# Optimization experiments

Hardware: AMD Instinct MI355X
Metric: run time of the kernel (lower is better)

Reference implementation:

```python
import jax, jax.numpy as jnp
import numpy as np
from jax.scipy.linalg import expm

U_SHAPE = (4, 32, 16, 16, 16, 3, 3)   # [mu, t, x, y, z, 3, 3]
W_SHAPE = (8, 32, 16, 16, 16, 3, 3)   # [feature, t, x, y, z, 3, 3]


def setup_inputs() -> dict:
    key = jax.random.key(0)
    k = jax.random.split(key, 5)
    return {
        "U_re": jax.random.normal(k[0], U_SHAPE, jnp.float32),
        "U_im": jax.random.normal(k[1], U_SHAPE, jnp.float32),
        "W_re": jax.random.normal(k[2], W_SHAPE, jnp.float32),
        "W_im": jax.random.normal(k[3], W_SHAPE, jnp.float32),
        "ah_weights": jax.random.normal(k[4], (4, W_SHAPE[0]), jnp.float32),
    }


def reference(U_re, U_im, W_re, W_im, ah_weights):
    U = (U_re + 1j * U_im).astype(jnp.complex64)
    W = (W_re + 1j * W_im).astype(jnp.complex64)

    # anti-hermitian part: W - W^dagger
    W_adj = jnp.conj(jnp.swapaxes(W, -1, -2))
    A = W - W_adj
    # traceless projection
    tr = jnp.trace(A, axis1=-2, axis2=-1)  # [i,t,x,y,z]
    A = A - (tr / 3.0)[..., None, None] * jnp.eye(3, dtype=A.dtype)

    # exponent: (1j*w) contracted with (-1j*A) == w contracted with A
    E = jnp.einsum('ui,itxyzab->utxyzab', ah_weights.astype(A.dtype), A)

    # batched 3x3 matrix exponential over the whole lattice
    E_flat = E.reshape(-1, 3, 3)
    expE = jax.vmap(expm)(E_flat).reshape(E.shape)

    # apply to gauge links: exp(...) @ U
    return jnp.einsum('utxyzij,utxyzjk->utxyzik', expE, U)
```

## Files before the change

kernel.cpp:

```cpp
#include <hip/hip_runtime.h>
#include <math.h>

#define NSITES 131072
#define HALFS  (NSITES / 2)
#define PL     (NSITES * 9)

struct cplx { float re, im; };

__device__ __forceinline__ cplx cadd(cplx a, cplx b) { return {a.re + b.re, a.im + b.im}; }
__device__ __forceinline__ cplx cmul(cplx a, cplx b) {
    return { fmaf(a.re, b.re, -(a.im * b.im)), fmaf(a.re, b.im, a.im * b.re) };
}

struct __attribute__((aligned(4))) f3 { float x, y, z; };
__device__ __forceinline__ f3 ld3(const float* __restrict__ p) { return *(const f3*)p; }
__device__ __forceinline__ void ld9(const float* __restrict__ p, float* r) {
    f3 a = *(const f3*)p, b = *(const f3*)(p + 3), c = *(const f3*)(p + 6);
    r[0] = a.x; r[1] = a.y; r[2] = a.z;
    r[3] = b.x; r[4] = b.y; r[5] = b.z;
    r[6] = c.x; r[7] = c.y; r[8] = c.z;
}

template<int IMM>
__device__ __forceinline__ void accf(const float* a, float wf, float* acc) {
    #pragma unroll
    for (int m = 0; m < 9; m++)
        acc[m] = fmaf(wf,
            __int_as_float(__builtin_amdgcn_ds_swizzle(__float_as_int(a[m]), IMM)),
            acc[m]);
}

__device__ __forceinline__ void prered(f3 q, f3 s, const float* wi, float* fr) {
    fr[0] = q.x - q.z;     fr[1] = q.y - s.y;     fr[2] = s.x - s.z;
    fr[3] = wi[1] + wi[3]; fr[4] = wi[2] + wi[6]; fr[5] = wi[5] + wi[7];
    fr[6] = wi[0];         fr[7] = wi[4];         fr[8] = wi[8];
}

struct Edof { float er01, er02, er12, ei01, ei02, ei12, ed0, ed1, ed2; };

__device__ __forceinline__ Edof make_edof(const float* acc) {
    Edof E;
    E.er01 = acc[0]; E.er02 = acc[1]; E.er12 = acc[2];
    E.ei01 = acc[3]; E.ei02 = acc[4]; E.ei12 = acc[5];
    float t3 = (acc[6] + acc[7] + acc[8]) * (2.f / 3.f);
    E.ed0 = fmaf(2.f, acc[6], -t3);
    E.ed1 = fmaf(2.f, acc[7], -t3);
    E.ed2 = fmaf(2.f, acc[8], -t3);
    return E;
}

__device__ __forceinline__ void expm_coeffs(const Edof& E, cplx& g0o, cplx& g1o, cplx& g2o)
{
    float r2 = fmaf(E.er01, E.er01, fmaf(E.er02, E.er02, fmaf(E.er12, E.er12,
               fmaf(E.ei01, E.ei01, fmaf(E.ei02, E.ei02, E.ei12 * E.ei12)))));
    r2 = fmaf(2.f, r2, fmaf(E.ed0, E.ed0, fmaf(E.ed1, E.ed1, E.ed2 * E.ed2)));

    const float n01 = fmaf(E.ei01, E.ei01, E.er01 * E.er01);
    const float n02 = fmaf(E.ei02, E.ei02, E.er02 * E.er02);
    const float n12 = fmaf(E.ei12, E.ei12, E.er12 * E.er12);
    const float zre = fmaf(E.ei01, E.ei12, -(E.er01 * E.er12));
    const float zim = -fmaf(E.ei01, E.er12, E.er01 * E.ei12);
    const float detH = E.ed0 * E.ed1 * E.ed2
                     + 2.f * fmaf(zre, E.ei02, -(zim * E.er02))
                     - fmaf(E.ed0, n12, fmaf(E.ed1, n02, E.ed2 * n01));

    int e; (void)frexpf(r2, &e);
    int sc = (e <= -2) ? 0 : min(1 + ((e + 1) >> 1), 40);
    const float inv  = __int_as_float((127 - sc) << 23);
    const float inv2 = inv * inv;
    const float px   = -0.5f * r2 * inv2;
    const float qxi  = -detH * (inv2 * inv);

    cplx T0 = {1.f, 0.f}, T1 = {0.f, 0.f}, T2 = {0.f, 0.f};
    cplx S0 = {1.f, 0.f}, S1 = {0.f, 0.f}, S2 = {0.f, 0.f};
    #pragma unroll
    for (int n = 1; n <= 10; n++) {
        float c  = 1.f / (float)n;
        float qc = qxi * c;
        cplx nT0 = { -qc * T2.im, qc * T2.re };
        cplx nT1 = { c * fmaf(px, T2.re, T0.re), c * fmaf(px, T2.im, T0.im) };
        cplx nT2 = { c * T1.re, c * T1.im };
        T0 = nT0; T1 = nT1; T2 = nT2;
        S0 = cadd(S0, T0); S1 = cadd(S1, T1); S2 = cadd(S2, T2);
    }

    const float q2 = 2.f * qxi;
    for (int k = 0; k < sc; k++) {
        cplx f0 = S0, f1 = S1, f2 = S2;
        cplx f12 = cmul(f1, f2);
        cplx f01 = cmul(f0, f1);
        cplx f02 = cmul(f0, f2);
        float f00re = fmaf(f0.re, f0.re, -(f0.im * f0.im)), f00im = 2.f * f0.re * f0.im;
        float f11re = fmaf(f1.re, f1.re, -(f1.im * f1.im)), f11im = 2.f * f1.re * f1.im;
        float f22re = fmaf(f2.re, f2.re, -(f2.im * f2.im)), f22im = 2.f * f2.re * f2.im;
        S0.re = fmaf(-q2, f12.im, f00re);
        S0.im = fmaf( q2, f12.re, f00im);
        S1.re = fmaf(-qxi, f22im, 2.f * fmaf(px, f12.re, f01.re));
        S1.im = fmaf( qxi, f22re, 2.f * fmaf(px, f12.im, f01.im));
        S2.re = fmaf(px, f22re, fmaf(2.f, f02.re, f11re));
        S2.im = fmaf(px, f22im, fmaf(2.f, f02.im, f11im));
    }
    g0o = S0;
    g1o = { S1.re * inv,  S1.im * inv  };
    g2o = { S2.re * inv2, S2.im * inv2 };
}

__device__ __forceinline__ void ecol(const Edof& E, cplx m0, cplx m1, cplx m2,
                                     cplx& v0, cplx& v1, cplx& v2)
{
    v0.re = fmaf(-E.ed0, m0.im, fmaf(E.er01, m1.re, fmaf(-E.ei01, m1.im, fmaf(E.er02, m2.re, -(E.ei02 * m2.im)))));
    v0.im = fmaf( E.ed0, m0.re, fmaf(E.er01, m1.im, fmaf( E.ei01, m1.re, fmaf(E.er02, m2.im,  (E.ei02 * m2.re)))));
    v1.re = fmaf(-E.er01, m0.re, fmaf(-E.ei01, m0.im, fmaf(-E.ed1, m1.im, fmaf(E.er12, m2.re, -(E.ei12 * m2.im)))));
    v1.im = fmaf(-E.er01, m0.im, fmaf( E.ei01, m0.re, fmaf( E.ed1, m1.re, fmaf(E.er12, m2.im,  (E.ei12 * m2.re)))));
    v2.re = fmaf(-E.er02, m0.re, fmaf(-E.ei02, m0.im, fmaf(-E.er12, m1.re, fmaf(-E.ei12, m1.im, -(E.ed2 * m2.im)))));
    v2.im = fmaf(-E.er02, m0.im, fmaf( E.ei02, m0.re, fmaf(-E.er12, m1.im, fmaf( E.ei12, m1.re,  (E.ed2 * m2.re)))));
}

__device__ __forceinline__ float ocomb(cplx g0, cplx g1, cplx g2, cplx m, cplx v, cplx z) {
    return fmaf(g0.re, m.re, fmaf(-g0.im, m.im, fmaf(g1.re, v.re, fmaf(-g1.im, v.im,
           fmaf(g2.re, z.re, -(g2.im * z.im))))));
}

__device__ __forceinline__ void apply_store(const Edof& E, cplx g0, cplx g1, cplx g2,
                                            const float* ur, const float* ui,
                                            float* __restrict__ ob)
{
    float o[9];
    #pragma unroll
    for (int b = 0; b < 3; b++) {
        cplx m0 = { ur[b],     ui[b]     };
        cplx m1 = { ur[3 + b], ui[3 + b] };
        cplx m2 = { ur[6 + b], ui[6 + b] };
        cplx v0, v1, v2, z0, z1, z2;
        ecol(E, m0, m1, m2, v0, v1, v2);
        ecol(E, v0, v1, v2, z0, z1, z2);
        o[b]     = ocomb(g0, g1, g2, m0, v0, z0);
        o[3 + b] = ocomb(g0, g1, g2, m1, v1, z1);
        o[6 + b] = ocomb(g0, g1, g2, m2, v2, z2);
    }
    *(f3*)(ob)     = { o[0], o[1], o[2] };
    *(f3*)(ob + 3) = { o[3], o[4], o[5] };
    *(f3*)(ob + 6) = { o[6], o[7], o[8] };
}

__global__ __launch_bounds__(256, 4) void lge_exp_kernel(
    const float* __restrict__ U_re, const float* __restrict__ U_im,
    const float* __restrict__ W_re, const float* __restrict__ W_im,
    const float* __restrict__ ahw,  float* __restrict__ out)
{
    const int gid = blockIdx.x * 256 + threadIdx.x;
    const int sA  = gid >> 2;
    const int mu  = gid & 3;
    const int sB  = sA + HALFS;

    const float4* ahw4 = (const float4*)ahw;
    float4 wlo = ahw4[mu * 2], whi = ahw4[mu * 2 + 1];
    const float wfv[8] = { wlo.x, wlo.y, wlo.z, wlo.w, whi.x, whi.y, whi.z, whi.w };

    const float* WrLo = W_re + (size_t)mu * PL;
    const float* WiLo = W_im + (size_t)mu * PL;
    const float* WrHi = W_re + (size_t)(mu + 4) * PL;
    const float* WiHi = W_im + (size_t)(mu + 4) * PL;
    const size_t bA = (size_t)sA * 9, bB = (size_t)sB * 9;

    f3 qAl = ld3(WrLo + bA + 1), sAl = ld3(WrLo + bA + 5);
    f3 qAh = ld3(WrHi + bA + 1), sAh = ld3(WrHi + bA + 5);
    f3 qBl = ld3(WrLo + bB + 1), sBl = ld3(WrLo + bB + 5);
    f3 qBh = ld3(WrHi + bB + 1), sBh = ld3(WrHi + bB + 5);
    float iAl[9]; ld9(WiLo + bA, iAl);
    float iAh[9]; ld9(WiHi + bA, iAh);
    float iBl[9]; ld9(WiLo + bB, iBl);
    float iBh[9]; ld9(WiHi + bB, iBh);

    float faA[9], fbA[9], faB[9], fbB[9];
    prered(qAl, sAl, iAl, faA);
    prered(qAh, sAh, iAh, fbA);
    prered(qBl, sBl, iBl, faB);
    prered(qBh, sBh, iBh, fbB);

    float accA[9] = {0.f,0.f,0.f,0.f,0.f,0.f,0.f,0.f,0.f};
    float accB[9] = {0.f,0.f,0.f,0.f,0.f,0.f,0.f,0.f,0.f};
    accf<0x1C>(faA, wfv[0], accA); accf<0x3C>(faA, wfv[1], accA);
    accf<0x5C>(faA, wfv[2], accA); accf<0x7C>(faA, wfv[3], accA);
    accf<0x1C>(fbA, wfv[4], accA); accf<0x3C>(fbA, wfv[5], accA);
    accf<0x5C>(fbA, wfv[6], accA); accf<0x7C>(fbA, wfv[7], accA);
    accf<0x1C>(faB, wfv[0], accB); accf<0x3C>(faB, wfv[1], accB);
    accf<0x5C>(faB, wfv[2], accB); accf<0x7C>(faB, wfv[3], accB);
    accf<0x1C>(fbB, wfv[4], accB); accf<0x3C>(fbB, wfv[5], accB);
    accf<0x5C>(fbB, wfv[6], accB); accf<0x7C>(fbB, wfv[7], accB);

    const Edof EA = make_edof(accA);
    const Edof EB = make_edof(accB);

    const size_t ubA = ((size_t)mu * NSITES + sA) * 9;
    float urA[9], uiA[9];
    ld9(U_re + ubA, urA); ld9(U_im + ubA, uiA);
    cplx g0A, g1A, g2A;
    expm_coeffs(EA, g0A, g1A, g2A);
    apply_store(EA, g0A, g1A, g2A, urA, uiA, out + ubA);

    const size_t ubB = ((size_t)mu * NSITES + sB) * 9;
    float urB[9], uiB[9];
    ld9(U_re + ubB, urB); ld9(U_im + ubB, uiB);
    cplx g0B, g1B, g2B;
    expm_coeffs(EB, g0B, g1B, g2B);
    apply_store(EB, g0B, g1B, g2B, urB, uiB, out + ubB);
}

extern "C" void kernel_launch(void* const* d_in, const int* in_sizes, int n_in,
                              void* d_out, int out_size, void* d_ws, size_t ws_size,
                              hipStream_t stream) {
    const float* U_re = (const float*)d_in[0];
    const float* U_im = (const float*)d_in[1];
    const float* W_re = (const float*)d_in[2];
    const float* W_im = (const float*)d_in[3];
    const float* ahw  = (const float*)d_in[4];
    float* out = (float*)d_out;
    lge_exp_kernel<<<dim3(NSITES * 4 / 2 / 256), dim3(256), 0, stream>>>(
        U_re, U_im, W_re, W_im, ahw, out);
}
```

Baseline: 157.2 us.

## Assign one site per thread and compute all four directions without swizzles

```diff
diff --git a/kernel.cpp b/kernel.cpp
--- a/kernel.cpp
+++ b/kernel.cpp
@@ -2,7 +2,6 @@
 #include <math.h>
 
 #define NSITES 131072
-#define HALFS  (NSITES / 2)
 #define PL     (NSITES * 9)
 
 struct cplx { float re, im; };
@@ -19,21 +18,6 @@
     r[0] = a.x; r[1] = a.y; r[2] = a.z;
     r[3] = b.x; r[4] = b.y; r[5] = b.z;
     r[6] = c.x; r[7] = c.y; r[8] = c.z;
-}
-
-template<int IMM>
-__device__ __forceinline__ void accf(const float* a, float wf, float* acc) {
-    #pragma unroll
-    for (int m = 0; m < 9; m++)
-        acc[m] = fmaf(wf,
-            __int_as_float(__builtin_amdgcn_ds_swizzle(__float_as_int(a[m]), IMM)),
-            acc[m]);
-}
-
-__device__ __forceinline__ void prered(f3 q, f3 s, const float* wi, float* fr) {
-    fr[0] = q.x - q.z;     fr[1] = q.y - s.y;     fr[2] = s.x - s.z;
-    fr[3] = wi[1] + wi[3]; fr[4] = wi[2] + wi[6]; fr[5] = wi[5] + wi[7];
-    fr[6] = wi[0];         fr[7] = wi[4];         fr[8] = wi[8];
 }
 
 struct Edof { float er01, er02, er12, ei01, ei02, ei12, ed0, ed1, ed2; };
@@ -148,63 +132,59 @@
     const float* __restrict__ W_re, const float* __restrict__ W_im,
     const float* __restrict__ ahw,  float* __restrict__ out)
 {
-    const int gid = blockIdx.x * 256 + threadIdx.x;
-    const int sA  = gid >> 2;
-    const int mu  = gid & 3;
-    const int sB  = sA + HALFS;
-
-    const float4* ahw4 = (const float4*)ahw;
-    float4 wlo = ahw4[mu * 2], whi = ahw4[mu * 2 + 1];
-    const float wfv[8] = { wlo.x, wlo.y, wlo.z, wlo.w, whi.x, whi.y, whi.z, whi.w };
-
-    const float* WrLo = W_re + (size_t)mu * PL;
-    const float* WiLo = W_im + (size_t)mu * PL;
-    const float* WrHi = W_re + (size_t)(mu + 4) * PL;
-    const float* WiHi = W_im + (size_t)(mu + 4) * PL;
-    const size_t bA = (size_t)sA * 9, bB = (size_t)sB * 9;
-
-    f3 qAl = ld3(WrLo + bA + 1), sAl = ld3(WrLo + bA + 5);
-    f3 qAh = ld3(WrHi + bA + 1), sAh = ld3(WrHi + bA + 5);
-    f3 qBl = ld3(WrLo + bB + 1), sBl = ld3(WrLo + bB + 5);
-    f3 qBh = ld3(WrHi + bB + 1), sBh = ld3(WrHi + bB + 5);
-    float iAl[9]; ld9(WiLo + bA, iAl);
-    float iAh[9]; ld9(WiHi + bA, iAh);
-    float iBl[9]; ld9(WiLo + bB, iBl);
-    float iBh[9]; ld9(WiHi + bB, iBh);
-
-    float faA[9], fbA[9], faB[9], fbB[9];
-    prered(qAl, sAl, iAl, faA);
-    prered(qAh, sAh, iAh, fbA);
-    prered(qBl, sBl, iBl, faB);
-    prered(qBh, sBh, iBh, fbB);
-
-    float accA[9] = {0.f,0.f,0.f,0.f,0.f,0.f,0.f,0.f,0.f};
-    float accB[9] = {0.f,0.f,0.f,0.f,0.f,0.f,0.f,0.f,0.f};
-    accf<0x1C>(faA, wfv[0], accA); accf<0x3C>(faA, wfv[1], accA);
-    accf<0x5C>(faA, wfv[2], accA); accf<0x7C>(faA, wfv[3], accA);
-    accf<0x1C>(fbA, wfv[4], accA); accf<0x3C>(fbA, wfv[5], accA);
-    accf<0x5C>(fbA, wfv[6], accA); accf<0x7C>(fbA, wfv[7], accA);
-    accf<0x1C>(faB, wfv[0], accB); accf<0x3C>(faB, wfv[1], accB);
-    accf<0x5C>(faB, wfv[2], accB); accf<0x7C>(faB, wfv[3], accB);
-    accf<0x1C>(fbB, wfv[4], accB); accf<0x3C>(fbB, wfv[5], accB);
-    accf<0x5C>(fbB, wfv[6], accB); accf<0x7C>(fbB, wfv[7], accB);
-
-    const Edof EA = make_edof(accA);
-    const Edof EB = make_edof(accB);
-
-    const size_t ubA = ((size_t)mu * NSITES + sA) * 9;
-    float urA[9], uiA[9];
-    ld9(U_re + ubA, urA); ld9(U_im + ubA, uiA);
-    cplx g0A, g1A, g2A;
-    expm_coeffs(EA, g0A, g1A, g2A);
-    apply_store(EA, g0A, g1A, g2A, urA, uiA, out + ubA);
-
-    const size_t ubB = ((size_t)mu * NSITES + sB) * 9;
-    float urB[9], uiB[9];
-    ld9(U_re + ubB, urB); ld9(U_im + ubB, uiB);
-    cplx g0B, g1B, g2B;
-    expm_coeffs(EB, g0B, g1B, g2B);
-    apply_store(EB, g0B, g1B, g2B, urB, uiB, out + ubB);
+    const int site = blockIdx.x * 256 + threadIdx.x;
+    const size_t sb = (size_t)site * 9;
+
+    float acc0[9] = {0,0,0,0,0,0,0,0,0};
+    float acc1[9] = {0,0,0,0,0,0,0,0,0};
+    float acc2[9] = {0,0,0,0,0,0,0,0,0};
+    float acc3[9] = {0,0,0,0,0,0,0,0,0};
+
+    #pragma unroll
+    for (int f = 0; f < 8; f++) {
+        const float* pr = W_re + (size_t)f * PL + sb;
+        const float* pi = W_im + (size_t)f * PL + sb;
+        f3 q = ld3(pr + 1);
+        f3 s = ld3(pr + 5);
+        float wi[9];
+        ld9(pi, wi);
+
+        float p0 = q.x - q.z;
+        float p1 = q.y - s.y;
+        float p2 = s.x - s.z;
+        float p3 = wi[1] + wi[3];
+        float p4 = wi[2] + wi[6];
+        float p5 = wi[5] + wi[7];
+        float p6 = wi[0], p7 = wi[4], p8 = wi[8];
+
+        const float w0 = ahw[0 * 8 + f], w1 = ahw[1 * 8 + f];
+        const float w2 = ahw[2 * 8 + f], w3 = ahw[3 * 8 + f];
+        acc0[0]=fmaf(w0,p0,acc0[0]); acc0[1]=fmaf(w0,p1,acc0[1]); acc0[2]=fmaf(w0,p2,acc0[2]);
+        acc0[3]=fmaf(w0,p3,acc0[3]); acc0[4]=fmaf(w0,p4,acc0[4]); acc0[5]=fmaf(w0,p5,acc0[5]);
+        acc0[6]=fmaf(w0,p6,acc0[6]); acc0[7]=fmaf(w0,p7,acc0[7]); acc0[8]=fmaf(w0,p8,acc0[8]);
+        acc1[0]=fmaf(w1,p0,acc1[0]); acc1[1]=fmaf(w1,p1,acc1[1]); acc1[2]=fmaf(w1,p2,acc1[2]);
+        acc1[3]=fmaf(w1,p3,acc1[3]); acc1[4]=fmaf(w1,p4,acc1[4]); acc1[5]=fmaf(w1,p5,acc1[5]);
+        acc1[6]=fmaf(w1,p6,acc1[6]); acc1[7]=fmaf(w1,p7,acc1[7]); acc1[8]=fmaf(w1,p8,acc1[8]);
+        acc2[0]=fmaf(w2,p0,acc2[0]); acc2[1]=fmaf(w2,p1,acc2[1]); acc2[2]=fmaf(w2,p2,acc2[2]);
+        acc2[3]=fmaf(w2,p3,acc2[3]); acc2[4]=fmaf(w2,p4,acc2[4]); acc2[5]=fmaf(w2,p5,acc2[5]);
+        acc2[6]=fmaf(w2,p6,acc2[6]); acc2[7]=fmaf(w2,p7,acc2[7]); acc2[8]=fmaf(w2,p8,acc2[8]);
+        acc3[0]=fmaf(w3,p0,acc3[0]); acc3[1]=fmaf(w3,p1,acc3[1]); acc3[2]=fmaf(w3,p2,acc3[2]);
+        acc3[3]=fmaf(w3,p3,acc3[3]); acc3[4]=fmaf(w3,p4,acc3[4]); acc3[5]=fmaf(w3,p5,acc3[5]);
+        acc3[6]=fmaf(w3,p6,acc3[6]); acc3[7]=fmaf(w3,p7,acc3[7]); acc3[8]=fmaf(w3,p8,acc3[8]);
+    }
+
+    const float* accs[4] = { acc0, acc1, acc2, acc3 };
+    #pragma unroll
+    for (int mu = 0; mu < 4; mu++) {
+        const size_t ub = ((size_t)mu * NSITES + site) * 9;
+        float ur[9], ui[9];
+        ld9(U_re + ub, ur);
+        ld9(U_im + ub, ui);
+        const Edof E = make_edof(accs[mu]);
+        cplx g0, g1, g2;
+        expm_coeffs(E, g0, g1, g2);
+        apply_store(E, g0, g1, g2, ur, ui, out + ub);
+    }
 }
 
 extern "C" void kernel_launch(void* const* d_in, const int* in_sizes, int n_in,
@@ -216,6 +196,6 @@
     const float* W_im = (const float*)d_in[3];
     const float* ahw  = (const float*)d_in[4];
     float* out = (float*)d_out;
-    lge_exp_kernel<<<dim3(NSITES * 4 / 2 / 256), dim3(256), 0, stream>>>(
+    lge_exp_kernel<<<dim3(NSITES / 256), dim3(256), 0, stream>>>(
         U_re, U_im, W_re, W_im, ahw, out);
 }
```

Result: slower. 174.7 us (+11.1%).
